# Kernel optimization log

Hardware: AMD Instinct MI355X
Metric: run time of the kernel (lower is better)

Reference implementation:

```python
import jax, jax.numpy as jnp
import numpy as np

N_HEAD = 16
ROPE_BASE = 10000.0


def _rope_cos_sin(T, head_dim, dtype):
    inv_freq = 1.0 / (ROPE_BASE ** (jnp.arange(0, head_dim, 2, dtype=jnp.float32) / head_dim))
    t = jnp.arange(T, dtype=jnp.float32)
    freqs = jnp.einsum('i,j->ij', t, inv_freq)           # (T, head_dim/2)
    emb = jnp.concatenate([freqs, freqs], axis=-1)        # (T, head_dim)
    return jnp.cos(emb).astype(dtype), jnp.sin(emb).astype(dtype)


def _rotate_half(x):
    x1, x2 = jnp.split(x, 2, axis=-1)
    return jnp.concatenate([-x2, x1], axis=-1)


def setup_inputs() -> dict:
    key = jax.random.key(0)
    k1, k2, k3 = jax.random.split(key, 3)
    B, T, C = 4, 2048, 1024
    x = jax.random.normal(k1, (B, T, C), dtype=jnp.float32)
    W_attn = jax.random.normal(k2, (C, 3 * C), dtype=jnp.float32) * (1.0 / np.sqrt(C))
    W_proj = jax.random.normal(k3, (C, C), dtype=jnp.float32) * (1.0 / np.sqrt(C))
    return {"x": x, "W_attn": W_attn, "W_proj": W_proj}


def reference(x, W_attn, W_proj):
    B, T, C = x.shape
    H = N_HEAD
    D = C // H
    qkv = x @ W_attn                                       # (B, T, 3C)
    q, k, v = jnp.split(qkv, 3, axis=-1)
    # (B, T, C) -> (B, H, T, D)
    q = q.reshape(B, T, H, D).transpose(0, 2, 1, 3)
    k = k.reshape(B, T, H, D).transpose(0, 2, 1, 3)
    v = v.reshape(B, T, H, D).transpose(0, 2, 1, 3)
    cos, sin = _rope_cos_sin(T, D, x.dtype)                # (T, D) each
    cos = cos[None, None]
    sin = sin[None, None]
    q = q * cos + _rotate_half(q) * sin
    k = k * cos + _rotate_half(k) * sin
    # bidirectional SDPA (no mask)
    scale = 1.0 / jnp.sqrt(jnp.asarray(D, dtype=x.dtype))
    scores = jnp.einsum('bhqd,bhkd->bhqk', q, k) * scale
    attn = jax.nn.softmax(scores, axis=-1)
    y = jnp.einsum('bhqk,bhkd->bhqd', attn, v)             # (B, H, T, D)
    y = y.transpose(0, 2, 1, 3).reshape(B, T, C)
    return y @ W_proj
```

## Files before the change

### kernel.cpp

```cpp
#include <hip/hip_runtime.h>
#include <math.h>

#define T_SEQ 2048
#define C_DIM 1024
#define H_NUM 16
#define D_DIM 64

typedef _Float16 f16x8 __attribute__((ext_vector_type(8)));
typedef _Float16 f16x4 __attribute__((ext_vector_type(4)));
typedef float    f32x4_t __attribute__((ext_vector_type(4)));

__global__ __launch_bounds__(256)
void ra_conv_f16(const float* __restrict__ src, _Float16* __restrict__ dst,
                 int n4) {
    int i = blockIdx.x * 256 + threadIdx.x;
    if (i >= n4) return;
    float4 v = reinterpret_cast<const float4*>(src)[i];
    f16x4 h = { (_Float16)v.x, (_Float16)v.y, (_Float16)v.z, (_Float16)v.w };
    reinterpret_cast<f16x4*>(dst)[i] = h;
}

__global__ __launch_bounds__(256)
void ra_transpose_conv(const float* __restrict__ W, _Float16* __restrict__ Wt,
                       int R, int C) {
    __shared__ _Float16 tile[64][68];
    const int tid = threadIdx.x;
    const int r0 = blockIdx.y * 64, c0 = blockIdx.x * 64;
#pragma unroll
    for (int i = 0; i < 4; ++i) {
        int s = tid + 256 * i;
        int r = s >> 4, cq = s & 15;
        float4 w = *reinterpret_cast<const float4*>(
            &W[(size_t)(r0 + r) * C + c0 + cq * 4]);
        f16x4 h = { (_Float16)w.x, (_Float16)w.y, (_Float16)w.z, (_Float16)w.w };
        *reinterpret_cast<f16x4*>(&tile[r][cq * 4]) = h;
    }
    __syncthreads();
#pragma unroll
    for (int i = 0; i < 4; ++i) {
        int s = tid + 256 * i;
        int c = s >> 4, rq = s & 15;
        f16x4 o = { tile[rq * 4 + 0][c], tile[rq * 4 + 1][c],
                    tile[rq * 4 + 2][c], tile[rq * 4 + 3][c] };
        *reinterpret_cast<f16x4*>(&Wt[(size_t)(c0 + c) * R + r0 + rq * 4]) = o;
    }
}

template <bool F16OUT>
__global__ __launch_bounds__(256)
void ra_gemm_f16(const _Float16* __restrict__ A, const _Float16* __restrict__ Bt,
                 void* __restrict__ Cout, int M, int N, int K) {
    __shared__ _Float16 AhS[128 * 32];
    __shared__ _Float16 BhS[128 * 32];

    const int tid  = threadIdx.x;
    const int lane = tid & 63;
    const int wave = tid >> 6;
    const int wm   = wave >> 1, wn = wave & 1;
    const int lq   = lane & 15;
    const int lg   = lane >> 4;
    const int row0 = blockIdx.y * 128;
    const int col0 = blockIdx.x * 128;

    f32x4_t acc[4][4];
#pragma unroll
    for (int i = 0; i < 4; ++i)
#pragma unroll
        for (int j = 0; j < 4; ++j) acc[i][j] = {0.f, 0.f, 0.f, 0.f};

    for (int k0 = 0; k0 < K; k0 += 32) {
        __syncthreads();
#pragma unroll
        for (int i = 0; i < 2; ++i) {
            int s = tid + 256 * i;
            int r = s >> 2, g = s & 3;
            *reinterpret_cast<f16x8*>(&AhS[r * 32 + g * 8]) =
                *reinterpret_cast<const f16x8*>(
                    &A[(size_t)(row0 + r) * K + k0 + g * 8]);
            *reinterpret_cast<f16x8*>(&BhS[r * 32 + g * 8]) =
                *reinterpret_cast<const f16x8*>(
                    &Bt[(size_t)(col0 + r) * K + k0 + g * 8]);
        }
        __syncthreads();

        f16x8 af[4], bf[4];
#pragma unroll
        for (int t = 0; t < 4; ++t) {
            af[t] = *reinterpret_cast<const f16x8*>(
                &AhS[(wm * 64 + t * 16 + lq) * 32 + lg * 8]);
            bf[t] = *reinterpret_cast<const f16x8*>(
                &BhS[(wn * 64 + t * 16 + lq) * 32 + lg * 8]);
        }
#pragma unroll
        for (int mt = 0; mt < 4; ++mt)
#pragma unroll
            for (int nt = 0; nt < 4; ++nt)
                acc[mt][nt] = __builtin_amdgcn_mfma_f32_16x16x32_f16(
                    af[mt], bf[nt], acc[mt][nt], 0, 0, 0);
    }

#pragma unroll
    for (int mt = 0; mt < 4; ++mt)
#pragma unroll
        for (int nt = 0; nt < 4; ++nt) {
            int c = col0 + wn * 64 + nt * 16 + lq;
#pragma unroll
            for (int r = 0; r < 4; ++r) {
                int rr = row0 + wm * 64 + mt * 16 + 4 * lg + r;
                if (F16OUT)
                    ((_Float16*)Cout)[(size_t)rr * N + c] =
                        (_Float16)acc[mt][nt][r];
                else
                    ((float*)Cout)[(size_t)rr * N + c] = acc[mt][nt][r];
            }
        }
}

__global__ __launch_bounds__(256)
void ra_rope_f16(_Float16* __restrict__ qkv, int total) {
    int idx = blockIdx.x * 256 + threadIdx.x;
    if (idx >= total) return;
    int j   = idx & 31;
    int h   = (idx >> 5) & 15;
    int mtx = (idx >> 9) & 1;
    int bt  = idx >> 10;
    int t   = bt & (T_SEQ - 1);

    float inv = exp2f(-(float)j * 0.41524101186092029f);
    float ang = (float)t * inv;
    float s, c;
    sincosf(ang, &s, &c);
    float scale = (mtx == 0) ? 0.125f : 1.0f;

    size_t base = (size_t)bt * 3072 + (size_t)mtx * 1024 + h * 64 + j;
    float q0 = (float)qkv[base];
    float q1 = (float)qkv[base + 32];
    qkv[base]      = (_Float16)((q0 * c - q1 * s) * scale);
    qkv[base + 32] = (_Float16)((q1 * c + q0 * s) * scale);
}

__global__ __launch_bounds__(256)
void ra_attn_mfma(const _Float16* __restrict__ qkv, _Float16* __restrict__ Y) {
    __shared__ __align__(16) unsigned char smem_raw[24576];
    _Float16* Ks = (_Float16*)smem_raw;
    _Float16* Vt = (_Float16*)(smem_raw + 8192);
    _Float16* Pt = (_Float16*)(smem_raw + 16384);

    const int tid  = threadIdx.x;
    const int lane = tid & 63;
    const int wave = tid >> 6;
    const int lq   = lane & 15;
    const int lg   = lane >> 4;
    const int swz  = (lq & 7) << 3;

    const int t0 = blockIdx.x * 64;
    const int h  = blockIdx.y;
    const int b  = blockIdx.z;

    const _Float16* Qg = qkv + (size_t)b * T_SEQ * 3072 + h * 64;
    const _Float16* Kg = Qg + 1024;
    const _Float16* Vg = Qg + 2048;

    f16x8 qf[2];
    {
        const _Float16* qrow = Qg + (size_t)(t0 + wave * 16 + lq) * 3072 + lg * 8;
        qf[0] = *reinterpret_cast<const f16x8*>(qrow);
        qf[1] = *reinterpret_cast<const f16x8*>(qrow + 32);
    }

    const f32x4_t vzero = {0.f, 0.f, 0.f, 0.f};
    float m_run = -1e30f, l_run = 0.f;
    f32x4_t o[4];
#pragma unroll
    for (int i = 0; i < 4; ++i) o[i] = vzero;

    const int dsub = tid & 15, kvq = tid >> 4;

    for (int kt = 0; kt < T_SEQ / 64; ++kt) {
        __syncthreads();
        const int kvb = kt * 64;
#pragma unroll
        for (int i = 0; i < 4; ++i) {
            int s  = tid + 256 * i;
            int kv = s >> 4, dq = s & 15;
            f16x4 hh = *reinterpret_cast<const f16x4*>(
                &Kg[(size_t)(kvb + kv) * 3072 + dq * 4]);
            *reinterpret_cast<f16x4*>(
                &Ks[kv * 64 + ((dq * 4) ^ ((kv & 7) << 3))]) = hh;
        }
#pragma unroll
        for (int i = 0; i < 4; ++i) {
            int d = dsub + 16 * i;
            const _Float16* vcol = &Vg[(size_t)(kvb + kvq * 4) * 3072 + d];
            f16x4 hh = { vcol[0], vcol[3072], vcol[6144], vcol[9216] };
            *reinterpret_cast<f16x4*>(
                &Vt[d * 64 + ((kvq * 4) ^ ((d & 7) << 3))]) = hh;
        }
        __syncthreads();

        f32x4_t st[4];
#pragma unroll
        for (int t = 0; t < 4; ++t) {
            st[t] = vzero;
#pragma unroll
            for (int mk = 0; mk < 2; ++mk) {
                f16x8 ak = *reinterpret_cast<const f16x8*>(
                    &Ks[(t * 16 + lq) * 64 + ((lg * 8 + mk * 32) ^ swz)]);
                st[t] = __builtin_amdgcn_mfma_f32_16x16x32_f16(
                    ak, qf[mk], st[t], 0, 0, 0);
            }
        }

        float mloc = -1e30f;
#pragma unroll
        for (int t = 0; t < 4; ++t)
#pragma unroll
            for (int r = 0; r < 4; ++r) mloc = fmaxf(mloc, st[t][r]);
        mloc = fmaxf(mloc, __shfl_xor(mloc, 16));
        mloc = fmaxf(mloc, __shfl_xor(mloc, 32));
        float mnew  = fmaxf(m_run, mloc);
        float alpha = __expf(m_run - mnew);
        float rs = 0.f;
        float p[4][4];
#pragma unroll
        for (int t = 0; t < 4; ++t)
#pragma unroll
            for (int r = 0; r < 4; ++r) {
                p[t][r] = __expf(st[t][r] - mnew);
                rs += p[t][r];
            }
        rs += __shfl_xor(rs, 16);
        rs += __shfl_xor(rs, 32);
        l_run = l_run * alpha + rs;
        m_run = mnew;
#pragma unroll
        for (int i = 0; i < 4; ++i) o[i] *= alpha;

        _Float16* Pw = Pt + wave * 1024 + lq * 64;
#pragma unroll
        for (int t = 0; t < 4; ++t) {
            f16x4 ph = { (_Float16)p[t][0], (_Float16)p[t][1],
                         (_Float16)p[t][2], (_Float16)p[t][3] };
            *reinterpret_cast<f16x4*>(&Pw[(t * 16 + lg * 4) ^ swz]) = ph;
        }
        __syncthreads();

        f16x8 bp[2];
#pragma unroll
        for (int mk = 0; mk < 2; ++mk)
            bp[mk] = *reinterpret_cast<const f16x8*>(
                &Pw[(lg * 8 + mk * 32) ^ swz]);
#pragma unroll
        for (int dt = 0; dt < 4; ++dt) {
#pragma unroll
            for (int mk = 0; mk < 2; ++mk) {
                f16x8 av = *reinterpret_cast<const f16x8*>(
                    &Vt[(dt * 16 + lq) * 64 + ((lg * 8 + mk * 32) ^ swz)]);
                o[dt] = __builtin_amdgcn_mfma_f32_16x16x32_f16(
                    av, bp[mk], o[dt], 0, 0, 0);
            }
        }
    }

    __syncthreads();
    float* Of = (float*)smem_raw;
    {
        float inv = 1.0f / l_run;
        int q = wave * 16 + lq;
#pragma unroll
        for (int dt = 0; dt < 4; ++dt)
#pragma unroll
            for (int r = 0; r < 4; ++r) {
                int d = dt * 16 + lg * 4 + r;
                Of[q * 64 + (d ^ ((q & 7) << 2))] = o[dt][r] * inv;
            }
    }
    __syncthreads();
#pragma unroll
    for (int i = 0; i < 4; ++i) {
        int s = tid + 256 * i;
        int row = s >> 4, dq = s & 15;
        float4 v = *reinterpret_cast<float4*>(
            &Of[row * 64 + ((dq * 4) ^ ((row & 7) << 2))]);
        f16x4 hv = { (_Float16)v.x, (_Float16)v.y, (_Float16)v.z, (_Float16)v.w };
        *reinterpret_cast<f16x4*>(
            &Y[((size_t)b * T_SEQ + t0 + row) * C_DIM + h * 64 + dq * 4]) = hv;
    }
}

extern "C" void kernel_launch(void* const* d_in, const int* in_sizes, int n_in,
                              void* d_out, int out_size, void* d_ws, size_t ws_size,
                              hipStream_t stream) {
    const float* x      = (const float*)d_in[0];
    const float* W_attn = (const float*)d_in[1];
    const float* W_proj = (const float*)d_in[2];
    float* out = (float*)d_out;

    const int B = in_sizes[0] / (T_SEQ * C_DIM);
    const int M = B * T_SEQ;

    unsigned char* ws = (unsigned char*)d_ws;
    _Float16* xh   = (_Float16*)(ws);
    _Float16* qkvh = (_Float16*)(ws + (16u << 20));
    _Float16* Yh   = (_Float16*)(ws + (64u << 20));
    _Float16* WaT  = (_Float16*)(ws + (80u << 20));
    _Float16* WpT  = (_Float16*)(ws + (86u << 20));

    int n4 = M * C_DIM / 4;
    hipLaunchKernelGGL(ra_conv_f16, dim3((n4 + 255) / 256), dim3(256), 0,
                       stream, x, xh, n4);

    hipLaunchKernelGGL(ra_transpose_conv, dim3(3 * C_DIM / 64, C_DIM / 64),
                       dim3(256), 0, stream, W_attn, WaT, C_DIM, 3 * C_DIM);
    hipLaunchKernelGGL(ra_transpose_conv, dim3(C_DIM / 64, C_DIM / 64),
                       dim3(256), 0, stream, W_proj, WpT, C_DIM, C_DIM);

    hipLaunchKernelGGL((ra_gemm_f16<true>), dim3(3 * C_DIM / 128, M / 128),
                       dim3(256), 0, stream, xh, WaT, (void*)qkvh,
                       M, 3 * C_DIM, C_DIM);

    int total = M * 2 * H_NUM * 32;
    hipLaunchKernelGGL(ra_rope_f16, dim3(total / 256), dim3(256), 0, stream,
                       qkvh, total);

    hipLaunchKernelGGL(ra_attn_mfma, dim3(T_SEQ / 64, H_NUM, B), dim3(256), 0,
                       stream, qkvh, Yh);

    hipLaunchKernelGGL((ra_gemm_f16<false>), dim3(C_DIM / 128, M / 128),
                       dim3(256), 0, stream, Yh, WpT, (void*)out,
                       M, C_DIM, C_DIM);
}
```

Before: 380.2 us.

## Use direct global-to-LDS loads in GEMM and read K straight from global in attention

The GEMM tile staging now uses global_load_lds builtins, which write global data straight into LDS without passing through registers. In the attention kernel the K tile is no longer staged in shared memory. Each wave reads its K fragments directly from global memory, which removes one LDS buffer and its writes, reads and swizzling. The cost is that every wave now refetches the same K rows from global/L2 instead of sharing one copy through LDS. The LDS write offsets in the GEMM must also land exactly where the existing fragment reads expect them.

```diff
diff --git a/kernel.cpp b/kernel.cpp
--- a/kernel.cpp
+++ b/kernel.cpp
@@ -74,12 +74,17 @@
         for (int i = 0; i < 2; ++i) {
             int s = tid + 256 * i;
             int r = s >> 2, g = s & 3;
-            *reinterpret_cast<f16x8*>(&AhS[r * 32 + g * 8]) =
-                *reinterpret_cast<const f16x8*>(
-                    &A[(size_t)(row0 + r) * K + k0 + g * 8]);
-            *reinterpret_cast<f16x8*>(&BhS[r * 32 + g * 8]) =
-                *reinterpret_cast<const f16x8*>(
-                    &Bt[(size_t)(col0 + r) * K + k0 + g * 8]);
+            const _Float16* ga = &A[(size_t)(row0 + r) * K + k0 + g * 8];
+            const _Float16* gb = &Bt[(size_t)(col0 + r) * K + k0 + g * 8];
+            int base = (wave * 64 + i * 256) * 16;
+            __builtin_amdgcn_global_load_lds(
+                (const __attribute__((address_space(1))) void*)ga,
+                (__attribute__((address_space(3))) void*)((char*)AhS + base),
+                16, 0, 0);
+            __builtin_amdgcn_global_load_lds(
+                (const __attribute__((address_space(1))) void*)gb,
+                (__attribute__((address_space(3))) void*)((char*)BhS + base),
+                16, 0, 0);
         }
         __syncthreads();
 
@@ -141,10 +146,9 @@
 
 __global__ __launch_bounds__(256)
 void ra_attn_mfma(const _Float16* __restrict__ qkv, _Float16* __restrict__ Y) {
-    __shared__ __align__(16) unsigned char smem_raw[24576];
-    _Float16* Ks = (_Float16*)smem_raw;
-    _Float16* Vt = (_Float16*)(smem_raw + 8192);
-    _Float16* Pt = (_Float16*)(smem_raw + 16384);
+    __shared__ __align__(16) unsigned char smem_raw[16384];
+    _Float16* Vt = (_Float16*)smem_raw;
+    _Float16* Pt = (_Float16*)(smem_raw + 8192);
 
     const int tid  = threadIdx.x;
     const int lane = tid & 63;
@@ -167,6 +171,7 @@
         qf[0] = *reinterpret_cast<const f16x8*>(qrow);
         qf[1] = *reinterpret_cast<const f16x8*>(qrow + 32);
     }
+    const _Float16* Kl = Kg + (size_t)lq * 3072 + lg * 8;
 
     const f32x4_t vzero = {0.f, 0.f, 0.f, 0.f};
     float m_run = -1e30f, l_run = 0.f;
@@ -179,15 +184,6 @@
     for (int kt = 0; kt < T_SEQ / 64; ++kt) {
         __syncthreads();
         const int kvb = kt * 64;
-#pragma unroll
-        for (int i = 0; i < 4; ++i) {
-            int s  = tid + 256 * i;
-            int kv = s >> 4, dq = s & 15;
-            f16x4 hh = *reinterpret_cast<const f16x4*>(
-                &Kg[(size_t)(kvb + kv) * 3072 + dq * 4]);
-            *reinterpret_cast<f16x4*>(
-                &Ks[kv * 64 + ((dq * 4) ^ ((kv & 7) << 3))]) = hh;
-        }
 #pragma unroll
         for (int i = 0; i < 4; ++i) {
             int d = dsub + 16 * i;
@@ -205,7 +201,7 @@
 #pragma unroll
             for (int mk = 0; mk < 2; ++mk) {
                 f16x8 ak = *reinterpret_cast<const f16x8*>(
-                    &Ks[(t * 16 + lq) * 64 + ((lg * 8 + mk * 32) ^ swz)]);
+                    Kl + (size_t)(kvb + t * 16) * 3072 + mk * 32);
                 st[t] = __builtin_amdgcn_mfma_f32_16x16x32_f16(
                     ak, qf[mk], st[t], 0, 0, 0);
             }
```

Result: slower. 509.8 us (+34.1%).
